# Kernel tuning notes

Measured on AMD Instinct MI355X. Metric: run time of the kernel, lower is better.

Reference implementation:

```python
import jax, jax.numpy as jnp
import numpy as np

D_MODEL = 768
D_FF = 2048
NUM_EXPERTS = 8
TOP_K = 2


def setup_inputs() -> dict:
    key = jax.random.key(0)
    ks = jax.random.split(key, 5)
    s_in = 1.0 / np.sqrt(D_MODEL)
    s_ff = 1.0 / np.sqrt(D_FF)
    x = jax.random.normal(ks[0], (2, 1024, D_MODEL), dtype=jnp.float32)
    gate_w = jax.random.normal(ks[1], (D_MODEL, NUM_EXPERTS), dtype=jnp.float32) * s_in
    w_gate = jax.random.normal(ks[2], (NUM_EXPERTS, D_MODEL, D_FF), dtype=jnp.float32) * s_in
    w_up = jax.random.normal(ks[3], (NUM_EXPERTS, D_MODEL, D_FF), dtype=jnp.float32) * s_in
    w_down = jax.random.normal(ks[4], (NUM_EXPERTS, D_FF, D_MODEL), dtype=jnp.float32) * s_ff
    return {"x": x, "gate_w": gate_w, "w_gate": w_gate, "w_up": w_up, "w_down": w_down}


def reference(x, gate_w, w_gate, w_up, w_down):
    B, S, D = x.shape
    xf = x.reshape(-1, D)  # [T, D]

    # Router (eval mode: no noise)
    logits = xf @ gate_w                      # [T, E]
    gates = jax.nn.softmax(logits, axis=-1)
    top_g, top_i = jax.lax.top_k(gates, TOP_K)             # [T, K]
    top_g = top_g / jnp.sum(top_g, axis=-1, keepdims=True)

    # combine weights: [T, E] = sum_k gate_k * onehot(idx_k)
    combine = jnp.sum(
        jax.nn.one_hot(top_i, NUM_EXPERTS, dtype=xf.dtype) * top_g[..., None], axis=1
    )

    # SwiGLU experts computed densely, masked/weighted by combine
    g = jnp.einsum("td,edf->etf", xf, w_gate)  # [E, T, F]
    u = jnp.einsum("td,edf->etf", xf, w_up)
    h = jax.nn.silu(g) * u
    eo = jnp.einsum("etf,efd->etd", h, w_down)  # [E, T, D]
    out = jnp.einsum("te,etd->td", combine, eo)  # [T, D]

    load_balancing_loss = jnp.asarray(0.0, dtype=xf.dtype)  # eval mode
    return out.reshape(B, S, D), load_balancing_loss
```

## Files before the change

kernel.cpp:

```cpp
#include <hip/hip_runtime.h>
#include <stdint.h>

typedef __attribute__((ext_vector_type(8))) short short8;
typedef __attribute__((ext_vector_type(4))) float f32x4;
typedef unsigned int u32;
typedef unsigned short u16;

#define T_TOK 2048
#define DMODEL 768
#define DFF 2048
#define NEXP 8

#define BKP 40
#define WSTR 20

#define M_CNT 0
#define M_CUR 8
#define M_OFF 16

#define G1_GRID 640
#define G1_PERX 80
#define G2_GRID 432
#define G2_PERX 54

#define PREP_WT 1152
#define PREP_RT (PREP_WT + 512)
#define PREP_GRID (PREP_RT + 384)

__device__ __forceinline__ float b2f(u16 u) {
  union { u32 i; float f; } v; v.i = ((u32)u) << 16; return v.f;
}
__device__ __forceinline__ u16 f2b(float f) {
  union { float f; u32 i; } v; v.f = f;
  return (u16)((v.i + 0x7fffu + ((v.i >> 16) & 1u)) >> 16);
}
__device__ __forceinline__ u32 pack2(float lo, float hi) {
  return (u32)f2b(lo) | ((u32)f2b(hi) << 16);
}
__device__ __forceinline__ uint4 cvt8(float4 a, float4 b) {
  uint4 r; r.x = pack2(a.x, a.y); r.y = pack2(a.z, a.w);
  r.z = pack2(b.x, b.y); r.w = pack2(b.z, b.w); return r;
}
__device__ __forceinline__ void gl16(const u16* g, u16* l) {
  __builtin_amdgcn_global_load_lds((const __attribute__((address_space(1))) void*)g,
                                   (__attribute__((address_space(3))) void*)l, 16, 0, 0);
}

__global__ __launch_bounds__(256) void k_prep(
    const float* __restrict__ wg, const float* __restrict__ wu, const float* __restrict__ wd,
    const float* __restrict__ x, const float* __restrict__ gw,
    u16* __restrict__ WgB, u16* __restrict__ WuB, u16* __restrict__ WdB,
    int* __restrict__ t2e, float* __restrict__ t2w, u16* __restrict__ xb,
    float* __restrict__ out) {
  int bid = blockIdx.x;
  int tid = threadIdx.x;
  if (bid < PREP_WT) {
    const float* in; u16* outw; int K, N, b;
    if (bid < 384) { in = wg; outw = WgB; K = 768; N = 2048; b = bid; }
    else if (bid < 768) { in = wu; outw = WuB; K = 768; N = 2048; b = bid - 384; }
    else { in = wd; outw = WdB; K = 2048; N = 768; b = bid - 768; }
    int e, nx, ky0;
    if (K == 768) {
      int t = (int)(((unsigned)b * 43691u) >> 17);
      int kc = b - t * 3;
      e = t >> 4; nx = t & 15; ky0 = kc * 8;
    } else {
      int kc = b & 7; int t = b >> 3;
      e = (int)(((unsigned)t * 43691u) >> 18);
      nx = t - e * 6; ky0 = kc * 8;
    }
    int nr = tid >> 1, kh = (tid & 1) * 16;
    const float* rp = in + (size_t)e * K * N + (size_t)(ky0 * 32 + kh) * N + nx * 128 + nr;
    int NB = N >> 7, KB = K >> 5;
    u16* op = outw + ((size_t)(e * NB + nx) * KB + ky0) * 4096 + nr * 32 + kh;
    size_t tstep = (size_t)32 * N;
#pragma unroll 1
    for (int i = 0; i < 8; ++i) {
      const float* rpi = rp + (size_t)i * tstep;
      float v[16];
#pragma unroll
      for (int j = 0; j < 16; ++j) v[j] = rpi[(size_t)j * N];
      uint4 o0, o1;
      o0.x = pack2(v[0], v[1]);  o0.y = pack2(v[2], v[3]);
      o0.z = pack2(v[4], v[5]);  o0.w = pack2(v[6], v[7]);
      o1.x = pack2(v[8], v[9]);  o1.y = pack2(v[10], v[11]);
      o1.z = pack2(v[12], v[13]); o1.w = pack2(v[14], v[15]);
      u16* opp = op + (size_t)i * 4096;
      *(uint4*)opp = o0;
      *(uint4*)(opp + 8) = o1;
    }
  } else if (bid < PREP_RT) {
    int lane = tid & 63;
    int t = (bid - PREP_WT) * 4 + (tid >> 6);
    const float* xr = x + (size_t)t * DMODEL;
    u16* xbr = xb + (size_t)t * DMODEL;
    float acc[8];
#pragma unroll
    for (int e = 0; e < 8; ++e) acc[e] = 0.f;
#pragma unroll
    for (int i = 0; i < 12; ++i) {
      int d = lane + (i << 6);
      float xd = xr[d];
      xbr[d] = f2b(xd);
      float4 g0 = *(const float4*)(gw + d * 8);
      float4 g1 = *(const float4*)(gw + d * 8 + 4);
      acc[0] += xd * g0.x; acc[1] += xd * g0.y;
      acc[2] += xd * g0.z; acc[3] += xd * g0.w;
      acc[4] += xd * g1.x; acc[5] += xd * g1.y;
      acc[6] += xd * g1.z; acc[7] += xd * g1.w;
    }
#pragma unroll
    for (int s = 32; s >= 1; s >>= 1) {
#pragma unroll
      for (int e = 0; e < 8; ++e) acc[e] += __shfl_xor(acc[e], s);
    }
    if (lane == 0) {
      int i0 = 0;
#pragma unroll
      for (int e = 1; e < 8; ++e) if (acc[e] > acc[i0]) i0 = e;
      int i1 = (i0 == 0) ? 1 : 0;
#pragma unroll
      for (int e = 0; e < 8; ++e) if (e != i0 && acc[e] > acc[i1]) i1 = e;
      float w0 = 1.f / (1.f + __expf(acc[i1] - acc[i0]));
      t2e[2 * t] = i0; t2e[2 * t + 1] = i1;
      t2w[2 * t] = w0; t2w[2 * t + 1] = 1.f - w0;
    }
  } else {
    int zid = bid - PREP_RT;
    float4 z = (float4){0.f, 0.f, 0.f, 0.f};
    float* p = out + ((size_t)zid * 256 + tid) * 16;
    *(float4*)p = z; *(float4*)(p + 4) = z;
    *(float4*)(p + 8) = z; *(float4*)(p + 12) = z;
  }
}

__global__ __launch_bounds__(1024) void k_scansc(
    const int* __restrict__ t2e, const float* __restrict__ t2w, int* __restrict__ meta,
    int* __restrict__ tok_of_row, int* __restrict__ slot_of, float* __restrict__ w_of_row,
    float* __restrict__ outp) {
  __shared__ int cnt[8], cur[8];
  int tid = threadIdx.x;
  if (tid < 8) cnt[tid] = 0;
  __syncthreads();
  int e0a[2], e1a[2];
#pragma unroll
  for (int j = 0; j < 2; ++j) {
    int t = tid + j * 1024;
    e0a[j] = t2e[2 * t]; e1a[j] = t2e[2 * t + 1];
    atomicAdd(&cnt[e0a[j]], 1); atomicAdd(&cnt[e1a[j]], 1);
  }
  __syncthreads();
  if (tid == 0) {
    int r = 0;
#pragma unroll 1
    for (int e = 0; e < NEXP; ++e) {
      int c = cnt[e];
      meta[M_CNT + e] = c; meta[M_OFF + e] = r; cur[e] = r; r += c;
    }
    meta[M_OFF + NEXP] = r;
    outp[(size_t)T_TOK * DMODEL] = 0.f;
  }
  __syncthreads();
#pragma unroll
  for (int j = 0; j < 2; ++j) {
    int t = tid + j * 1024;
    int s0 = atomicAdd(&cur[e0a[j]], 1);
    tok_of_row[s0] = t; slot_of[2 * t] = s0; w_of_row[s0] = t2w[2 * t];
    int s1 = atomicAdd(&cur[e1a[j]], 1);
    tok_of_row[s1] = t; slot_of[2 * t + 1] = s1; w_of_row[s1] = t2w[2 * t + 1];
  }
}

__global__ __launch_bounds__(256, 3) void k_stage1b(
    const u16* __restrict__ Xb, const u16* __restrict__ WgB, const u16* __restrict__ WuB,
    const int* __restrict__ meta, const int* __restrict__ tok, u16* __restrict__ H) {
  __shared__ u16 Xs[2][4096];
  __shared__ u16 Wgs[2][4096];
  __shared__ u16 Wus[2][4096];
  int bid = blockIdx.x;
  int wid = (bid & 7) * G1_PERX + (bid >> 3);
  int e = 0, base = 0, Te = 0, off_e = 0, rows_e = 0;
#pragma unroll 1
  for (e = 0; e < NEXP; ++e) {
    off_e = meta[M_OFF + e];
    rows_e = meta[M_OFF + e + 1] - off_e;
    Te = (rows_e + 127) >> 7;
    int c = Te << 4;
    if (wid < base + c) break;
    base += c;
  }
  if (e == NEXP) return;
  int local = wid - base;
  int rb = local >> 4, fb = local & 15;
  int r0 = rb * 128;
  int rows_t = rows_e - r0; if (rows_t > 128) rows_t = 128;
  int f0 = fb * 128;
  int tid = threadIdx.x, lane = tid & 63, w = tid >> 6;
  int wr = w >> 1, wc = w & 1, q = lane >> 4, lm = lane & 15;

  int rsub = lane >> 2;
  int g4 = (lane & 3) ^ ((lane >> 3) & 3);
  int rA = w * 32 + rsub;
  int cA = (rA < rows_t) ? rA : (rows_t - 1);
  int cB = (rA + 16 < rows_t) ? (rA + 16) : (rows_t - 1);
  const u16* aG0 = Xb + (size_t)tok[off_e + r0 + cA] * DMODEL + g4 * 8;
  const u16* aG1 = Xb + (size_t)tok[off_e + r0 + cB] * DMODEL + g4 * 8;
  size_t cb = (size_t)((e * 16 + fb) * 24) * 4096 + w * 1024 + rsub * 32 + g4 * 8;
  const u16* gG = WgB + cb;
  const u16* uG = WuB + cb;

  int qx = (q ^ ((lm >> 1) & 3)) * 8;
  int aoff = (wr * 64 + lm) * 32 + qx;
  int boff = (wc * 64 + lm) * 32 + qx;

  f32x4 accg[4][4], accu[4][4];
#pragma unroll
  for (int i = 0; i < 4; ++i)
#pragma unroll
    for (int j = 0; j < 4; ++j) {
      accg[i][j] = (f32x4){0.f, 0.f, 0.f, 0.f};
      accu[i][j] = (f32x4){0.f, 0.f, 0.f, 0.f};
    }

  auto STG = [&](int b, int kko) {
    int ka = kko * 32;
    size_t kb = (size_t)kko * 4096;
    gl16(aG0 + ka, &Xs[b][w * 1024]);
    gl16(aG1 + ka, &Xs[b][w * 1024 + 512]);
    gl16(gG + kb, &Wgs[b][w * 1024]);
    gl16(gG + kb + 512, &Wgs[b][w * 1024 + 512]);
    gl16(uG + kb, &Wus[b][w * 1024]);
    gl16(uG + kb + 512, &Wus[b][w * 1024 + 512]);
  };
  auto CMP = [&](int b) {
    const u16* ap = &Xs[b][aoff];
    const u16* gp = &Wgs[b][boff];
    const u16* up = &Wus[b][boff];
    short8 af[4];
#pragma unroll
    for (int mt = 0; mt < 4; ++mt) af[mt] = *(const short8*)(ap + mt * 512);
#pragma unroll
    for (int nt = 0; nt < 4; ++nt) {
      short8 bg = *(const short8*)(gp + nt * 512);
      short8 bu = *(const short8*)(up + nt * 512);
#pragma unroll
      for (int mt = 0; mt < 4; ++mt) {
        accg[mt][nt] = __builtin_amdgcn_mfma_f32_16x16x32_bf16(af[mt], bg, accg[mt][nt], 0, 0, 0);
        accu[mt][nt] = __builtin_amdgcn_mfma_f32_16x16x32_bf16(af[mt], bu, accu[mt][nt], 0, 0, 0);
      }
    }
  };

  STG(0, 0);
  for (int kko = 0; kko < 23; ++kko) {
    STG((kko + 1) & 1, kko + 1);
    asm volatile("s_waitcnt vmcnt(6)" ::: "memory");
    __builtin_amdgcn_s_barrier();
    asm volatile("" ::: "memory");
    CMP(kko & 1);
    asm volatile("s_waitcnt lgkmcnt(0)" ::: "memory");
    __builtin_amdgcn_s_barrier();
    asm volatile("" ::: "memory");
  }
  asm volatile("s_waitcnt vmcnt(0)" ::: "memory");
  __builtin_amdgcn_s_barrier();
  asm volatile("" ::: "memory");
  CMP(1);

#pragma unroll
  for (int mt = 0; mt < 4; ++mt)
#pragma unroll
    for (int r = 0; r < 4; ++r) {
      int lrow = wr * 64 + mt * 16 + q * 4 + r;
      if (lrow < rows_t) {
        size_t rowbase = (size_t)(off_e + r0 + lrow) * DFF + f0 + wc * 64;
#pragma unroll
        for (int nt = 0; nt < 4; ++nt) {
          float g = accg[mt][nt][r], u = accu[mt][nt][r];
          float h = g / (1.f + __expf(-g)) * u;
          H[rowbase + nt * 16 + lm] = f2b(h);
        }
      }
    }
}

__global__ __launch_bounds__(256, 3) void k_stage2b(
    const u16* __restrict__ H, const u16* __restrict__ WdB,
    const int* __restrict__ meta, const int* __restrict__ tok,
    const float* __restrict__ wrow, float* __restrict__ out) {
  __shared__ u16 As[2][4096];
  __shared__ u16 Ws[2][8192];
  int bid = blockIdx.x;
  int wid = (bid & 7) * G2_PERX + (bid >> 3);
  int e = 0, base = 0, off_e = 0, rows_e = 0;
#pragma unroll 1
  for (e = 0; e < NEXP; ++e) {
    off_e = meta[M_OFF + e];
    rows_e = meta[M_OFF + e + 1] - off_e;
    int Tr = (rows_e + 63) >> 6;
    int c = Tr * 6;
    if (wid < base + c) break;
    base += c;
  }
  if (e == NEXP) return;
  int local = wid - base;
  int rb = (int)(((unsigned)local * 43691u) >> 18);
  int nb = local - rb * 6;
  int r0 = rb * 64;
  int rows_t = rows_e - r0; if (rows_t > 64) rows_t = 64;
  int n0 = nb * 128;
  int tid = threadIdx.x, lane = tid & 63, w = tid >> 6;
  int q = lane >> 4, lm = lane & 15;

  int rsub = lane >> 2;
  int g4 = (lane & 3) ^ ((lane >> 3) & 3);
  int rA = w * 16 + rsub;
  int cA = (rA < rows_t) ? rA : (rows_t - 1);
  const u16* aG = H + (size_t)(off_e + r0 + cA) * DFF + g4 * 8;
  size_t cb = (size_t)((e * 6 + nb) * 64) * 4096 + w * 1024 + rsub * 32 + g4 * 8;
  const u16* wG = WdB + cb;

  int qx = (q ^ ((lm >> 1) & 3)) * 8;
  int aoff = lm * 32 + qx;
  int boff = (w * 32 + lm) * 32 + qx;

  f32x4 acc[4][2];
#pragma unroll
  for (int i = 0; i < 4; ++i)
#pragma unroll
    for (int j = 0; j < 2; ++j) acc[i][j] = (f32x4){0.f, 0.f, 0.f, 0.f};

  auto STG = [&](int b, int kko) {
    int ka = kko * 64;
    size_t kb = (size_t)kko * 8192;
    gl16(aG + ka, &As[b][w * 512]);
    gl16(aG + ka + 32, &As[b][2048 + w * 512]);
    gl16(wG + kb, &Ws[b][w * 1024]);
    gl16(wG + kb + 512, &Ws[b][w * 1024 + 512]);
    gl16(wG + kb + 4096, &Ws[b][4096 + w * 1024]);
    gl16(wG + kb + 4608, &Ws[b][4096 + w * 1024 + 512]);
  };
  auto CMP = [&](int b) {
    const u16* ap = &As[b][aoff];
    const u16* bp = &Ws[b][boff];
#pragma unroll
    for (int s = 0; s < 2; ++s) {
      short8 af[4];
#pragma unroll
      for (int mt = 0; mt < 4; ++mt) af[mt] = *(const short8*)(ap + s * 2048 + mt * 512);
#pragma unroll
      for (int nt = 0; nt < 2; ++nt) {
        short8 bb = *(const short8*)(bp + s * 4096 + nt * 512);
#pragma unroll
        for (int mt = 0; mt < 4; ++mt)
          acc[mt][nt] = __builtin_amdgcn_mfma_f32_16x16x32_bf16(af[mt], bb, acc[mt][nt], 0, 0, 0);
      }
    }
  };

  STG(0, 0);
  for (int kko = 0; kko < 31; ++kko) {
    STG((kko + 1) & 1, kko + 1);
    asm volatile("s_waitcnt vmcnt(6)" ::: "memory");
    __builtin_amdgcn_s_barrier();
    asm volatile("" ::: "memory");
    CMP(kko & 1);
    asm volatile("s_waitcnt lgkmcnt(0)" ::: "memory");
    __builtin_amdgcn_s_barrier();
    asm volatile("" ::: "memory");
  }
  asm volatile("s_waitcnt vmcnt(0)" ::: "memory");
  __builtin_amdgcn_s_barrier();
  asm volatile("" ::: "memory");
  CMP(1);

#pragma unroll
  for (int mt = 0; mt < 4; ++mt)
#pragma unroll
    for (int r = 0; r < 4; ++r) {
      int lrow = mt * 16 + q * 4 + r;
      if (lrow < rows_t) {
        int row = off_e + r0 + lrow;
        int token = tok[row];
        float wgt = wrow[row];
        float* ob = out + (size_t)token * DMODEL + n0 + w * 32;
#pragma unroll
        for (int nt = 0; nt < 2; ++nt)
          atomicAdd(&ob[nt * 16 + lm], wgt * acc[mt][nt][r]);
      }
    }
}

__global__ __launch_bounds__(192) void k_combine(
    const float* __restrict__ Op, const int* __restrict__ slot_of,
    const float* __restrict__ t2w, float* __restrict__ out) {
  int t = blockIdx.x;
  int d4 = threadIdx.x << 2;
  int s0 = slot_of[2 * t], s1 = slot_of[2 * t + 1];
  float w0 = t2w[2 * t], w1 = t2w[2 * t + 1];
  float4 a = *(const float4*)&Op[(size_t)s0 * DMODEL + d4];
  float4 b = *(const float4*)&Op[(size_t)s1 * DMODEL + d4];
  float4 r;
  r.x = w0 * a.x + w1 * b.x;
  r.y = w0 * a.y + w1 * b.y;
  r.z = w0 * a.z + w1 * b.z;
  r.w = w0 * a.w + w1 * b.w;
  *(float4*)&out[(size_t)t * DMODEL + d4] = r;
}

__global__ __launch_bounds__(256) void k_router_fb(
    const float* __restrict__ x, const float* __restrict__ gw,
    int* __restrict__ t2e, float* __restrict__ t2w, u16* __restrict__ xb) {
  int lane = threadIdx.x & 63;
  int t = blockIdx.x * 4 + (threadIdx.x >> 6);
  const float* xr = x + (size_t)t * DMODEL;
  u16* xbr = xb + (size_t)t * DMODEL;
  float acc[8];
#pragma unroll
  for (int e = 0; e < 8; ++e) acc[e] = 0.f;
#pragma unroll
  for (int i = 0; i < 12; ++i) {
    int d = lane + (i << 6);
    float xd = xr[d];
    xbr[d] = f2b(xd);
    float4 g0 = *(const float4*)(gw + d * 8);
    float4 g1 = *(const float4*)(gw + d * 8 + 4);
    acc[0] += xd * g0.x; acc[1] += xd * g0.y;
    acc[2] += xd * g0.z; acc[3] += xd * g0.w;
    acc[4] += xd * g1.x; acc[5] += xd * g1.y;
    acc[6] += xd * g1.z; acc[7] += xd * g1.w;
  }
#pragma unroll
  for (int s = 32; s >= 1; s >>= 1) {
#pragma unroll
    for (int e = 0; e < 8; ++e) acc[e] += __shfl_xor(acc[e], s);
  }
  if (lane == 0) {
    int i0 = 0;
#pragma unroll
    for (int e = 1; e < 8; ++e) if (acc[e] > acc[i0]) i0 = e;
    int i1 = (i0 == 0) ? 1 : 0;
#pragma unroll
    for (int e = 0; e < 8; ++e) if (e != i0 && acc[e] > acc[i1]) i1 = e;
    float w0 = 1.f / (1.f + __expf(acc[i1] - acc[i0]));
    t2e[2 * t] = i0; t2e[2 * t + 1] = i1;
    t2w[2 * t] = w0; t2w[2 * t + 1] = 1.f - w0;
  }
}

__device__ __forceinline__ void wpack(u32* lds, int k2, int n8, uint4 a, uint4 b) {
  int idx = n8 * WSTR + k2;
  lds[idx + 0 * WSTR] = (a.x & 0xffffu) | (b.x << 16);
  lds[idx + 1 * WSTR] = (a.x >> 16) | (b.x & 0xffff0000u);
  lds[idx + 2 * WSTR] = (a.y & 0xffffu) | (b.y << 16);
  lds[idx + 3 * WSTR] = (a.y >> 16) | (b.y & 0xffff0000u);
  lds[idx + 4 * WSTR] = (a.z & 0xffffu) | (b.z << 16);
  lds[idx + 5 * WSTR] = (a.z >> 16) | (b.z & 0xffff0000u);
  lds[idx + 6 * WSTR] = (a.w & 0xffffu) | (b.w << 16);
  lds[idx + 7 * WSTR] = (a.w >> 16) | (b.w & 0xffff0000u);
}

__global__ __launch_bounds__(256) void k_stage1f(
    const float* __restrict__ xv, const float* __restrict__ wgv, const float* __restrict__ wuv,
    const int* __restrict__ meta, const int* __restrict__ tok, u16* __restrict__ H) {
  __shared__ u16 Xs[64 * 32];
  __shared__ u16 Wgs[128 * BKP];
  __shared__ u16 Wus[128 * BKP];
  int e = blockIdx.z;
  int off_e = meta[M_OFF + e];
  int rows_e = meta[M_OFF + e + 1] - off_e;
  int r0 = blockIdx.y * 64;
  if (r0 >= rows_e) return;
  int rows_t = rows_e - r0; if (rows_t > 64) rows_t = 64;
  int f0 = blockIdx.x * 128;
  int tid = threadIdx.x, lane = tid & 63, w = tid >> 6;
  int wr = w >> 1, wc = w & 1;
  int srow = (w << 4) + (lane >> 2);
  int trow = (srow < rows_t) ? tok[off_e + r0 + srow] : tok[off_e];
  int xcol = (lane & 3) << 3;
  u16* xl = &Xs[srow * 32 + xcol];
  int k2 = tid >> 4, n8 = (tid & 15) << 3;
  size_t wbase = (size_t)e * (DMODEL * DFF) + (size_t)(k2 << 1) * DFF + f0 + n8;
  f32x4 accg[2][4], accu[2][4];
#pragma unroll
  for (int i = 0; i < 2; ++i)
#pragma unroll
    for (int j = 0; j < 4; ++j) {
      accg[i][j] = (f32x4){0.f, 0.f, 0.f, 0.f};
      accu[i][j] = (f32x4){0.f, 0.f, 0.f, 0.f};
    }
  for (int kk = 0; kk < DMODEL / 32; ++kk) {
    int k0 = kk << 5;
    const float* xg = xv + (size_t)trow * DMODEL + xcol;
    const float* wgp = wgv + wbase;
    const float* wup = wuv + wbase;
    uint4 xa = cvt8(*(const float4*)(xg + k0), *(const float4*)(xg + k0 + 4));
    uint4 ga = cvt8(*(const float4*)(wgp + (size_t)k0 * DFF), *(const float4*)(wgp + (size_t)k0 * DFF + 4));
    uint4 gb = cvt8(*(const float4*)(wgp + (size_t)k0 * DFF + DFF), *(const float4*)(wgp + (size_t)k0 * DFF + DFF + 4));
    uint4 ua = cvt8(*(const float4*)(wup + (size_t)k0 * DFF), *(const float4*)(wup + (size_t)k0 * DFF + 4));
    uint4 ub = cvt8(*(const float4*)(wup + (size_t)k0 * DFF + DFF), *(const float4*)(wup + (size_t)k0 * DFF + DFF + 4));
    __syncthreads();
    *(uint4*)xl = xa;
    wpack((u32*)Wgs, k2, n8, ga, gb);
    wpack((u32*)Wus, k2, n8, ua, ub);
    __syncthreads();
    short8 af[2];
#pragma unroll
    for (int mt = 0; mt < 2; ++mt)
      af[mt] = *(const short8*)&Xs[((wr << 5) + (mt << 4) + (lane & 15)) * 32 + ((lane >> 4) << 3)];
#pragma unroll
    for (int nt = 0; nt < 4; ++nt) {
      int col = (wc << 6) + (nt << 4) + (lane & 15);
      short8 bg = *(const short8*)&Wgs[col * BKP + ((lane >> 4) << 3)];
      short8 bu = *(const short8*)&Wus[col * BKP + ((lane >> 4) << 3)];
#pragma unroll
      for (int mt = 0; mt < 2; ++mt) {
        accg[mt][nt] = __builtin_amdgcn_mfma_f32_16x16x32_bf16(af[mt], bg, accg[mt][nt], 0, 0, 0);
        accu[mt][nt] = __builtin_amdgcn_mfma_f32_16x16x32_bf16(af[mt], bu, accu[mt][nt], 0, 0, 0);
      }
    }
  }
  int q = lane >> 4, c = lane & 15;
#pragma unroll
  for (int mt = 0; mt < 2; ++mt)
#pragma unroll
    for (int r = 0; r < 4; ++r) {
      int lrow = (wr << 5) + (mt << 4) + (q << 2) + r;
      if (lrow < rows_t) {
        size_t rowbase = (size_t)(off_e + r0 + lrow) * DFF + f0 + (wc << 6);
#pragma unroll
        for (int nt = 0; nt < 4; ++nt) {
          float g = accg[mt][nt][r], u = accu[mt][nt][r];
          float h = g / (1.f + __expf(-g)) * u;
          H[rowbase + (nt << 4) + c] = f2b(h);
        }
      }
    }
}

__global__ __launch_bounds__(256) void k_stage2f(
    const u16* __restrict__ H, const float* __restrict__ wdv,
    const int* __restrict__ meta, float* __restrict__ Op) {
  __shared__ u16 As[64 * 32];
  __shared__ u16 Ws[128 * BKP];
  int e = blockIdx.z;
  int off_e = meta[M_OFF + e];
  int rows_e = meta[M_OFF + e + 1] - off_e;
  int r0 = blockIdx.y * 64;
  if (r0 >= rows_e) return;
  int rows_t = rows_e - r0; if (rows_t > 64) rows_t = 64;
  int n0 = blockIdx.x * 128;
  int tid = threadIdx.x, lane = tid & 63, w = tid >> 6;
  int wr = w >> 1, wc = w & 1;
  int srow = (w << 4) + (lane >> 2);
  int hrow = off_e + r0 + ((srow < rows_t) ? srow : 0);
  const u16* ag = H + (size_t)hrow * DFF + ((lane & 3) << 3);
  u16* al = &As[srow * 32 + ((lane & 3) << 3)];
  int k2 = tid >> 4, n8 = (tid & 15) << 3;
  size_t wbase = (size_t)e * (DFF * DMODEL) + (size_t)(k2 << 1) * DMODEL + n0 + n8;
  f32x4 acc[2][4];
#pragma unroll
  for (int i = 0; i < 2; ++i)
#pragma unroll
    for (int j = 0; j < 4; ++j) acc[i][j] = (f32x4){0.f, 0.f, 0.f, 0.f};
  for (int kk = 0; kk < DFF / 32; ++kk) {
    int k0 = kk << 5;
    uint4 xa = *(const uint4*)(ag + k0);
    const float* wdp = wdv + wbase;
    uint4 ga = cvt8(*(const float4*)(wdp + (size_t)k0 * DMODEL), *(const float4*)(wdp + (size_t)k0 * DMODEL + 4));
    uint4 gb = cvt8(*(const float4*)(wdp + (size_t)k0 * DMODEL + DMODEL), *(const float4*)(wdp + (size_t)k0 * DMODEL + DMODEL + 4));
    __syncthreads();
    *(uint4*)al = xa;
    wpack((u32*)Ws, k2, n8, ga, gb);
    __syncthreads();
    short8 af[2];
#pragma unroll
    for (int mt = 0; mt < 2; ++mt)
      af[mt] = *(const short8*)&As[((wr << 5) + (mt << 4) + (lane & 15)) * 32 + ((lane >> 4) << 3)];
#pragma unroll
    for (int nt = 0; nt < 4; ++nt) {
      int col = (wc << 6) + (nt << 4) + (lane & 15);
      short8 b = *(const short8*)&Ws[col * BKP + ((lane >> 4) << 3)];
#pragma unroll
      for (int mt = 0; mt < 2; ++mt)
        acc[mt][nt] = __builtin_amdgcn_mfma_f32_16x16x32_bf16(af[mt], b, acc[mt][nt], 0, 0, 0);
    }
  }
  int q = lane >> 4, c = lane & 15;
#pragma unroll
  for (int mt = 0; mt < 2; ++mt)
#pragma unroll
    for (int r = 0; r < 4; ++r) {
      int lrow = (wr << 5) + (mt << 4) + (q << 2) + r;
      if (lrow < rows_t) {
        size_t rowbase = (size_t)(off_e + r0 + lrow) * DMODEL + n0 + (wc << 6);
#pragma unroll
        for (int nt = 0; nt < 4; ++nt)
          Op[rowbase + (nt << 4) + c] = acc[mt][nt][r];
      }
    }
}

extern "C" void kernel_launch(void* const* d_in, const int* in_sizes, int n_in,
                              void* d_out, int out_size, void* d_ws, size_t ws_size,
                              hipStream_t stream) {
  const float* x  = (const float*)d_in[0];
  const float* gw = (const float*)d_in[1];
  const float* wg = (const float*)d_in[2];
  const float* wu = (const float*)d_in[3];
  const float* wd = (const float*)d_in[4];
  float* out = (float*)d_out;

  char* ws = (char*)d_ws;
  int* meta = (int*)ws;
  int* t2e        = (int*)(ws + 256);
  int* slot_of    = (int*)(ws + 16640);
  int* tok_of_row = (int*)(ws + 33024);
  float* t2w      = (float*)(ws + 49408);
  u16* Xb         = (u16*)(ws + 65792);

  const size_t NEED = 108069120;
  if (ws_size >= NEED) {
    u16* H         = (u16*)(ws + 3211520);
    float* w_of_row = (float*)(ws + 19988736);
    u16* WgB   = (u16*)(ws + 32571648);
    u16* WuB   = (u16*)(ws + 57737472);
    u16* WdB   = (u16*)(ws + 82903296);

    k_prep<<<PREP_GRID, 256, 0, stream>>>(wg, wu, wd, x, gw, WgB, WuB, WdB,
                                          t2e, t2w, Xb, out);
    k_scansc<<<1, 1024, 0, stream>>>(t2e, t2w, meta, tok_of_row, slot_of, w_of_row, out);
    k_stage1b<<<G1_GRID, 256, 0, stream>>>(Xb, WgB, WuB, meta, tok_of_row, H);
    k_stage2b<<<G2_GRID, 256, 0, stream>>>(H, WdB, meta, tok_of_row, w_of_row, out);
  } else {
    u16* H    = (u16*)(ws + 65792);
    float* Op = (float*)(ws + 65792 + 16777216);
    float* w_of_row = (float*)(ws + 65792 + 16777216 + 12582912);
    k_router_fb<<<T_TOK / 4, 256, 0, stream>>>(x, gw, t2e, t2w, Xb);
    k_scansc<<<1, 1024, 0, stream>>>(t2e, t2w, meta, tok_of_row, slot_of, w_of_row, out);
    dim3 g1(DFF / 128, T_TOK / 64, NEXP);
    k_stage1f<<<g1, 256, 0, stream>>>(x, wg, wu, meta, tok_of_row, H);
    dim3 g2(DMODEL / 128, T_TOK / 64, NEXP);
    k_stage2f<<<g2, 256, 0, stream>>>(H, wd, meta, Op);
    k_combine<<<T_TOK, 192, 0, stream>>>(Op, slot_of, t2w, out);
  }
}
```

Baseline: 291.5 us.

## Stage weight-transpose tiles through LDS with double-buffered async global loads

The weight conversion section of the prep kernel used to read fp32 weights column-strided straight from global memory. It now fetches 32x128 fp32 tiles with coalesced 16-byte global_load_lds into a double-buffered shared array. The transpose and bf16 pack are then done from LDS, with the next tiles prefetched while the current one is processed. This adds manual vmcnt waits and barriers, plus 32KB of shared memory per block, which could reduce occupancy for the other prep branches.

```diff
diff --git a/kernel.cpp b/kernel.cpp
--- a/kernel.cpp
+++ b/kernel.cpp
@@ -42,6 +42,10 @@
   r.z = pack2(b.x, b.y); r.w = pack2(b.z, b.w); return r;
 }
 __device__ __forceinline__ void gl16(const u16* g, u16* l) {
+  __builtin_amdgcn_global_load_lds((const __attribute__((address_space(1))) void*)g,
+                                   (__attribute__((address_space(3))) void*)l, 16, 0, 0);
+}
+__device__ __forceinline__ void gl16f(const float* g, float* l) {
   __builtin_amdgcn_global_load_lds((const __attribute__((address_space(1))) void*)g,
                                    (__attribute__((address_space(3))) void*)l, 16, 0, 0);
 }
@@ -52,6 +56,7 @@
     u16* __restrict__ WgB, u16* __restrict__ WuB, u16* __restrict__ WdB,
     int* __restrict__ t2e, float* __restrict__ t2w, u16* __restrict__ xb,
     float* __restrict__ out) {
+  __shared__ float TB[2][4096];
   int bid = blockIdx.x;
   int tid = threadIdx.x;
   if (bid < PREP_WT) {
@@ -69,17 +74,30 @@
       e = (int)(((unsigned)t * 43691u) >> 18);
       nx = t - e * 6; ky0 = kc * 8;
     }
+    int lane = tid & 63, w = tid >> 6;
+    const float* src = in + (size_t)e * K * N
+                     + (size_t)(ky0 * 32 + w * 8 + (lane >> 5)) * N
+                     + nx * 128 + ((lane & 31) << 2);
     int nr = tid >> 1, kh = (tid & 1) * 16;
-    const float* rp = in + (size_t)e * K * N + (size_t)(ky0 * 32 + kh) * N + nx * 128 + nr;
     int NB = N >> 7, KB = K >> 5;
     u16* op = outw + ((size_t)(e * NB + nx) * KB + ky0) * 4096 + nr * 32 + kh;
-    size_t tstep = (size_t)32 * N;
+    auto STGW = [&](int bf, int i) {
+#pragma unroll
+      for (int j = 0; j < 4; ++j)
+        gl16f(src + (size_t)(i * 32 + 2 * j) * N, &TB[bf][w * 1024 + j * 256]);
+    };
+    STGW(0, 0); STGW(1, 1);
 #pragma unroll 1
     for (int i = 0; i < 8; ++i) {
-      const float* rpi = rp + (size_t)i * tstep;
+      if (i == 0)      asm volatile("s_waitcnt vmcnt(4)" ::: "memory");
+      else if (i < 7)  asm volatile("s_waitcnt vmcnt(6)" ::: "memory");
+      else             asm volatile("s_waitcnt vmcnt(2)" ::: "memory");
+      __builtin_amdgcn_s_barrier();
+      asm volatile("" ::: "memory");
+      const float* Tb = TB[i & 1];
       float v[16];
 #pragma unroll
-      for (int j = 0; j < 16; ++j) v[j] = rpi[(size_t)j * N];
+      for (int j = 0; j < 16; ++j) v[j] = Tb[(kh + j) * 128 + nr];
       uint4 o0, o1;
       o0.x = pack2(v[0], v[1]);  o0.y = pack2(v[2], v[3]);
       o0.z = pack2(v[4], v[5]);  o0.w = pack2(v[6], v[7]);
@@ -88,6 +106,10 @@
       u16* opp = op + (size_t)i * 4096;
       *(uint4*)opp = o0;
       *(uint4*)(opp + 8) = o1;
+      asm volatile("s_waitcnt lgkmcnt(0)" ::: "memory");
+      __builtin_amdgcn_s_barrier();
+      asm volatile("" ::: "memory");
+      if (i + 2 < 8) STGW(i & 1, i + 2);
     }
   } else if (bid < PREP_RT) {
     int lane = tid & 63;
```

Result: faster. 268.3 us (-8.0%).
